# Kernel optimization log

Measured on AMD Instinct MI355X. Metric: run time of the kernel, lower is better.

## Reference

```python
import jax, jax.numpy as jnp
import numpy as np

B, H, W, C = 32, 64, 64, 64
F = 128
KH = KW = 3
SH = SW = 1
P = KH * KW * C  # flattened patch size = 576


def _glorot(key, shape):
    fan_in = KH * KW * C
    fan_out = KH * KW * F
    limit = np.sqrt(6.0 / (fan_in + fan_out)).astype(np.float32)
    return jax.random.uniform(key, shape, jnp.float32, -limit, limit)


def setup_inputs() -> dict:
    key = jax.random.key(0)
    k1, k2, k3 = jax.random.split(key, 3)
    inputs = jax.random.normal(k1, (B, H, W, C), dtype=jnp.float32)
    kernel = _glorot(k2, (KH, KW, C, F))
    control_points = _glorot(k3, (KH, KW, C, F))
    bias = jnp.zeros((F,), dtype=jnp.float32)
    return {"inputs": inputs, "kernel": kernel, "bias": bias, "control_points": control_points}


def _extract_patches(x):
    # SAME padding, stride 1; TF extract_patches ordering: (kh, kw, C), C fastest
    xp = jnp.pad(x, ((0, 0), (1, 1), (1, 1), (0, 0)))
    patches = jnp.stack(
        [xp[:, i:i + H, j:j + W, :] for i in range(KH) for j in range(KW)],
        axis=3,
    )  # [B, H, W, KH*KW, C]
    return patches.reshape(B, H, W, P)


def reference(inputs, kernel, bias, control_points):
    conv_out = jax.lax.conv_general_dilated(
        inputs, kernel, (SH, SW), "SAME",
        dimension_numbers=("NHWC", "HWIO", "NHWC"),
    )  # [B, H, W, F]

    # RBF branch via ||a-b||^2 = ||a||^2 + ||b||^2 - 2 a.b
    p = _extract_patches(inputs).reshape(-1, P)        # [N, P]
    c = control_points.reshape(P, F)                   # [P, F]
    pn = jnp.sum(p * p, axis=1, keepdims=True)         # [N, 1]
    cn = jnp.sum(c * c, axis=0)                        # [F]
    d = pn + cn - 2.0 * (p @ c)                        # [N, F] squared distances
    gamma = 1.0 / (2.0 * jnp.mean(d))                  # global mean over all patches/filters
    kan = jnp.exp(-gamma * d).reshape(B, H, W, F)

    return conv_out + kan + bias
```

## Files before the change

kernel.cpp:

```cpp
#include <hip/hip_runtime.h>


#define B_ 32
#define H_ 64
#define W_ 64
#define C_ 64
#define F_ 128
#define P_ 576
#define NPIX (B_*H_*W_)
#define NF   (NPIX*F_)

typedef __bf16  bf16x8 __attribute__((ext_vector_type(8)));
typedef float   f32x4  __attribute__((ext_vector_type(4)));

union FU  { float f; uint u; };
union BFU { __bf16 h; ushort s; };
union PKU { __bf16 h[2]; uint u; };

__device__ __forceinline__ ushort f2bf(float f) { BFU q; q.h = (__bf16)f; return q.s; }
__device__ __forceinline__ uint pk(float a, float b) {
    PKU q; q.h[0] = (__bf16)a; q.h[1] = (__bf16)b; return q.u;
}
__device__ __forceinline__ float bflo(uint u) { FU v; v.u = u << 16; return v.f; }
__device__ __forceinline__ float bfhi(uint u) { FU v; v.u = u & 0xffff0000u; return v.f; }

__device__ __forceinline__ void gll16(const void* g, void* l) {
    __builtin_amdgcn_global_load_lds((const __attribute__((address_space(1))) void*)g,
                                     (__attribute__((address_space(3))) void*)l, 16, 0, 0);
}

#define ACC_SPN 0
#define ACC_SPC 16
#define ACC_SCN 32

__global__ void k_prep(const float* __restrict__ wgt, const float* __restrict__ ctrl,
                       ushort* __restrict__ wsB, float* __restrict__ cn,
                       float* __restrict__ accum, float* __restrict__ tab) {
    __shared__ __attribute__((aligned(16))) float sh[1024];
    if (blockIdx.x < 288) {
        int e = blockIdx.x * 256 + threadIdx.x;
        int p = e >> 7, f = e & 127;
        int kc = p >> 6, r = p & 63;
        int ks = r >> 5, quad = (r >> 3) & 3, j = r & 7;
        int ntg = f >> 4, l16 = f & 15;
        int off0 = (kc * 2 + ks) * 8192 + ntg * 512 + (quad * 16 + l16) * 8 + j;
        wsB[off0]        = f2bf(wgt[e]);
        wsB[off0 + 4096] = f2bf(ctrl[e]);
    } else if (blockIdx.x == 288) {
        int t = threadIdx.x;
        int col = t & 31, pc = t >> 5;
        f32x4 a = {0.f, 0.f, 0.f, 0.f};
        const float* base = ctrl + col * 4;
        #pragma unroll 4
        for (int p = pc * 72; p < pc * 72 + 72; ++p) {
            f32x4 v = *(const f32x4*)(base + p * F_);
            a += v * v;
        }
        f32x4* sh4 = (f32x4*)sh;
        sh4[t] = a;
        __syncthreads();
        f32x4 s = {0.f, 0.f, 0.f, 0.f};
        if (t < 32) {
            #pragma unroll
            for (int q = 0; q < 8; ++q) s += sh4[q * 32 + t];
            *(f32x4*)(cn + t * 4) = s;
        }
        float tot = s.x + s.y + s.z + s.w;
        if (t < 64) {
            #pragma unroll
            for (int off = 32; off >= 1; off >>= 1) tot += __shfl_down(tot, off, 64);
            if (t == 0) {
                accum[ACC_SPN] = 0.f;
                accum[ACC_SPC] = 0.f;
                accum[ACC_SCN] = tot;
            }
        }
    } else {
        int t = threadIdx.x;
        for (int e = t; e < 576; e += 256) {
            const f32x4* row = (const f32x4*)(ctrl + e * F_);
            f32x4 a = {0.f, 0.f, 0.f, 0.f};
            #pragma unroll 8
            for (int q = 0; q < 32; ++q) a += row[q];
            sh[e] = a.x + a.y + a.z + a.w;
        }
        __syncthreads();
        for (int idx = t; idx < 576; idx += 256) {
            int q = idx >> 6, c = idx & 63;
            int ry = q / 3, rx = q - 3 * ry;
            int my = (ry == 0) ? 3 : (ry == 2) ? 6 : 7;
            int mx = (rx == 0) ? 3 : (rx == 2) ? 6 : 7;
            float s = 0.f;
            #pragma unroll
            for (int ki = 0; ki < 3; ++ki)
                #pragma unroll
                for (int kj = 0; kj < 3; ++kj)
                    if ((my >> ki & 1) && (mx >> kj & 1))
                        s += sh[(ki * 3 + kj) * 64 + c];
            tab[idx] = s;
        }
    }
}

__launch_bounds__(256)
__global__ void k_gamma(const float* __restrict__ in, const float* __restrict__ tab,
                        float* __restrict__ accum) {
    __shared__ float shs[4], shp[4];
    const int t = threadIdx.x, seg = t & 15, grp = t >> 4;
    float s = 0.f, pc = 0.f;
    #pragma unroll 4
    for (int it = 0; it < 16; ++it) {
        int pix = blockIdx.x * 256 + it * 16 + grp;
        int y = (pix >> 6) & 63, x = pix & 63;
        float4 v = *((const float4*)(in + pix * 64) + seg);
        int ry = (y == 0) ? 0 : (y == 63) ? 2 : 1;
        int rx = (x == 0) ? 0 : (x == 63) ? 2 : 1;
        float4 tv = *((const float4*)(tab + (ry * 3 + rx) * 64) + seg);
        float wq = (float)((3 - (y == 0) - (y == 63)) * (3 - (x == 0) - (x == 63)));
        s  += wq * (v.x*v.x + v.y*v.y + v.z*v.z + v.w*v.w);
        pc += v.x*tv.x + v.y*tv.y + v.z*tv.z + v.w*tv.w;
    }
    #pragma unroll
    for (int off = 32; off >= 1; off >>= 1) {
        s  += __shfl_down(s,  off, 64);
        pc += __shfl_down(pc, off, 64);
    }
    if ((t & 63) == 0) { shs[t >> 6] = s; shp[t >> 6] = pc; }
    __syncthreads();
    if (t == 0)  atomicAdd(&accum[ACC_SPN], shs[0] + shs[1] + shs[2] + shs[3]);
    if (t == 64) atomicAdd(&accum[ACC_SPC], shp[0] + shp[1] + shp[2] + shp[3]);
}

__launch_bounds__(512, 4)
__global__ void k_main(const float* __restrict__ in, const ushort* __restrict__ wsB,
                       const float* __restrict__ bias, const float* __restrict__ cn,
                       const float* __restrict__ accum, float* __restrict__ out) {
    __shared__ __attribute__((aligned(16))) ushort smem[34592];
    ushort* lI   = smem;
    ushort* lB   = smem + 17408;
    float*  sArr = (float*)(smem + 33792);
    float*  pnAr = (float*)(smem + 34336);

    const int tid = threadIdx.x;
    const int n0  = blockIdx.x * 128;
    const int b   = n0 >> 12;
    const int y0  = (n0 >> 6) & 63;
    const float* inb = in + b * 262144;

    const int w     = tid >> 6, lane = tid & 63;
    const int fq    = w & 3, mhalf = w >> 2;
    const int quad  = lane >> 4, l16 = lane & 15;

    {
        const char* src = (const char*)wsB + tid * 16;
        char* dst = (char*)lB + tid * 16;
        gll16(src, dst);
        gll16(src + 8192, dst + 8192);
    }

    for (int g = tid; g < 2176; g += 512) {
        int row4 = g / 544;
        int rem  = g - row4 * 544;
        int px = rem >> 3, c = rem & 7;
        int y = y0 + row4 - 1, x = px - 1;
        float4 v0 = make_float4(0.f, 0.f, 0.f, 0.f), v1 = v0;
        if (y >= 0 && y < 64 && x >= 0 && x < 64) {
            const float* sp = inb + y * 4096 + x * 64 + c * 8;
            v0 = *(const float4*)sp;
            v1 = *(const float4*)(sp + 4);
        }
        uint4 o = { pk(v0.x, v0.y), pk(v0.z, v0.w), pk(v1.x, v1.y), pk(v1.z, v1.w) };
        *(uint4*)&lI[(row4 * 68 + px) * 64 + ((c ^ (px & 7)) << 3)] = o;
    }
    __syncthreads();

    for (int g = tid; g < 264; g += 512) {
        int row4 = g / 66, px = g - row4 * 66;
        const ushort* base = &lI[(row4 * 68 + px) * 64];
        float s = 0.f;
        #pragma unroll
        for (int j = 0; j < 8; ++j) {
            int jj = (j + px) & 7;
            uint4 v = *(const uint4*)&base[jj << 3];
            float a0 = bflo(v.x), a1 = bfhi(v.x), a2 = bflo(v.y), a3 = bfhi(v.y);
            float a4 = bflo(v.z), a5 = bfhi(v.z), a6 = bflo(v.w), a7 = bfhi(v.w);
            s += a0*a0 + a1*a1 + a2*a2 + a3*a3 + a4*a4 + a5*a5 + a6*a6 + a7*a7;
        }
        sArr[row4 * 66 == 0 ? 0 : 0] = 0.f;
        sArr[row4 * 68 + px] = s;
    }
    __syncthreads();

    if (tid < 128) {
        int yr = tid >> 6, x = tid & 63;
        float a = 0.f;
        #pragma unroll
        for (int dr = 0; dr < 3; ++dr)
            #pragma unroll
            for (int dc = 0; dc < 3; ++dc)
                a += sArr[(yr + dr) * 68 + x + dc];
        pnAr[tid] = a;
    }

    f32x4 accW[4][2], accC[4][2];
    #pragma unroll
    for (int mt = 0; mt < 4; ++mt)
        #pragma unroll
        for (int nt = 0; nt < 2; ++nt) {
            accW[mt][nt] = (f32x4){0.f, 0.f, 0.f, 0.f};
            accC[mt][nt] = (f32x4){0.f, 0.f, 0.f, 0.f};
        }

    const int fq2 = fq * 2;
    int cur = 0;
    #pragma unroll 1
    for (int t18 = 0; t18 < 18; ++t18) {
        const int kc = t18 >> 1, ks = t18 & 1;
        const int ki = (kc >= 6) ? 2 : (kc >= 3) ? 1 : 0;
        const int kj = kc - 3 * ki;

        if (t18 < 17) {
            const char* src = (const char*)wsB + (t18 + 1) * 16384 + tid * 16;
            char* dst = (char*)lB + ((cur ^ 1) * 16384) + tid * 16;
            gll16(src, dst);
            gll16(src + 8192, dst + 8192);
        }

        const ushort* lBc = lB + cur * 8192;
        bf16x8 bw[2], bc[2];
        #pragma unroll
        for (int nt = 0; nt < 2; ++nt) {
            bw[nt] = *(const bf16x8*)&lBc[(fq2 + nt) * 512 + lane * 8];
            bc[nt] = *(const bf16x8*)&lBc[4096 + (fq2 + nt) * 512 + lane * 8];
        }
        const int swk = (l16 + kj) & 7;
        const int rb0 = (mhalf + ki) * 68 + l16 + kj;
        const int sw  = ((ks * 4 + quad) ^ swk) << 3;
        #pragma unroll
        for (int mt = 0; mt < 4; ++mt) {
            bf16x8 a = *(const bf16x8*)&lI[(rb0 + mt * 16) * 64 + sw];
            #pragma unroll
            for (int nt = 0; nt < 2; ++nt) {
                accW[mt][nt] = __builtin_amdgcn_mfma_f32_16x16x32_bf16(a, bw[nt], accW[mt][nt], 0, 0, 0);
                accC[mt][nt] = __builtin_amdgcn_mfma_f32_16x16x32_bf16(a, bc[nt], accC[mt][nt], 0, 0, 0);
            }
        }
        __syncthreads();
        cur ^= 1;
    }

    float Spn = accum[ACC_SPN], Spc = accum[ACC_SPC], Scn = accum[ACC_SCN];
    float Sd  = 128.f * Spn + 131072.f * Scn - 2.f * Spc;
    float g   = 0.5f * 16777216.f / Sd;
    float bv[2], cv[2];
    #pragma unroll
    for (int nt = 0; nt < 2; ++nt) {
        int gf = fq * 32 + nt * 16 + l16;
        bv[nt] = bias[gf];
        cv[nt] = cn[gf];
    }
    #pragma unroll
    for (int mt = 0; mt < 4; ++mt) {
        int rloc = mhalf * 64 + mt * 16 + quad * 4;
        float pv[4];
        #pragma unroll
        for (int r = 0; r < 4; ++r) pv[r] = pnAr[rloc + r];
        int gm = n0 + rloc;
        #pragma unroll
        for (int nt = 0; nt < 2; ++nt) {
            int gf = fq * 32 + nt * 16 + l16;
            #pragma unroll
            for (int r = 0; r < 4; ++r) {
                float d = pv[r] + cv[nt] - 2.f * accC[mt][nt][r];
                out[(gm + r) * F_ + gf] = accW[mt][nt][r] + bv[nt] + __expf(-g * d);
            }
        }
    }
}

extern "C" void kernel_launch(void* const* d_in, const int* in_sizes, int n_in,
                              void* d_out, int out_size, void* d_ws, size_t ws_size,
                              hipStream_t stream) {
    const float* in   = (const float*)d_in[0];
    const float* wgt  = (const float*)d_in[1];
    const float* bias = (const float*)d_in[2];
    const float* ctrl = (const float*)d_in[3];
    float* out = (float*)d_out;

    char* ws = (char*)d_ws;
    ushort* wsB   = (ushort*)(ws + 0);
    float*  cn    = (float*) (ws + 294912);
    float*  accum = (float*) (ws + 295424);
    float*  tab   = (float*) (ws + 295616);

    k_prep  <<<290,        256, 0, stream>>>(wgt, ctrl, wsB, cn, accum, tab);
    k_gamma <<<NPIX / 256, 256, 0, stream>>>(in, tab, accum);
    k_main  <<<NPIX / 128, 512, 0, stream>>>(in, wsB, bias, cn, accum, out);
}
```

Measured before the change: 146.8 us.

## Fuse gamma reduction into prep kernel and replace atomics with per-block partials

Merges the gamma-statistics kernel into the prep kernel as extra blocks, so one launch goes away. Each stats block now rebuilds the border table in LDS and writes per-block partial sums instead of doing atomics, and the main kernel reduces all 512 partials itself. The main kernel also computes the per-pixel squared norms during the LDS fill using shuffles, which removes a separate LDS pass and barrier. It skips the final-iteration barrier and raises wave priority around the MFMA block. The cost is that every stats block recomputes the 576-entry table redundantly, and every main wave reads 1024 partials.

```diff
diff --git a/kernel.cpp b/kernel.cpp
--- a/kernel.cpp
+++ b/kernel.cpp
@@ -13,7 +13,6 @@
 typedef __bf16  bf16x8 __attribute__((ext_vector_type(8)));
 typedef float   f32x4  __attribute__((ext_vector_type(4)));
 
-union FU  { float f; uint u; };
 union BFU { __bf16 h; ushort s; };
 union PKU { __bf16 h[2]; uint u; };
 
@@ -21,24 +20,23 @@
 __device__ __forceinline__ uint pk(float a, float b) {
     PKU q; q.h[0] = (__bf16)a; q.h[1] = (__bf16)b; return q.u;
 }
-__device__ __forceinline__ float bflo(uint u) { FU v; v.u = u << 16; return v.f; }
-__device__ __forceinline__ float bfhi(uint u) { FU v; v.u = u & 0xffff0000u; return v.f; }
 
 __device__ __forceinline__ void gll16(const void* g, void* l) {
     __builtin_amdgcn_global_load_lds((const __attribute__((address_space(1))) void*)g,
                                      (__attribute__((address_space(3))) void*)l, 16, 0, 0);
 }
 
-#define ACC_SPN 0
-#define ACC_SPC 16
-#define ACC_SCN 32
-
-__global__ void k_prep(const float* __restrict__ wgt, const float* __restrict__ ctrl,
-                       ushort* __restrict__ wsB, float* __restrict__ cn,
-                       float* __restrict__ accum, float* __restrict__ tab) {
+__global__ void k_prep(const float* __restrict__ in, const float* __restrict__ wgt,
+                       const float* __restrict__ ctrl, ushort* __restrict__ wsB,
+                       float* __restrict__ cn, float* __restrict__ accum,
+                       float* __restrict__ spn, float* __restrict__ spc) {
     __shared__ __attribute__((aligned(16))) float sh[1024];
+    __shared__ float tabL[576];
+    __shared__ float shs[4], shp[4];
+    const int t = threadIdx.x;
+
     if (blockIdx.x < 288) {
-        int e = blockIdx.x * 256 + threadIdx.x;
+        int e = blockIdx.x * 256 + t;
         int p = e >> 7, f = e & 127;
         int kc = p >> 6, r = p & 63;
         int ks = r >> 5, quad = (r >> 3) & 3, j = r & 7;
@@ -46,13 +44,14 @@
         int off0 = (kc * 2 + ks) * 8192 + ntg * 512 + (quad * 16 + l16) * 8 + j;
         wsB[off0]        = f2bf(wgt[e]);
         wsB[off0 + 4096] = f2bf(ctrl[e]);
-    } else if (blockIdx.x == 288) {
-        int t = threadIdx.x;
-        int col = t & 31, pc = t >> 5;
+        return;
+    }
+    if (blockIdx.x == 288) {
+        int col = t & 31, pc8 = t >> 5;
         f32x4 a = {0.f, 0.f, 0.f, 0.f};
         const float* base = ctrl + col * 4;
         #pragma unroll 4
-        for (int p = pc * 72; p < pc * 72 + 72; ++p) {
+        for (int p = pc8 * 72; p < pc8 * 72 + 72; ++p) {
             f32x4 v = *(const f32x4*)(base + p * F_);
             a += v * v;
         }
@@ -69,53 +68,46 @@
         if (t < 64) {
             #pragma unroll
             for (int off = 32; off >= 1; off >>= 1) tot += __shfl_down(tot, off, 64);
-            if (t == 0) {
-                accum[ACC_SPN] = 0.f;
-                accum[ACC_SPC] = 0.f;
-                accum[ACC_SCN] = tot;
-            }
-        }
-    } else {
-        int t = threadIdx.x;
-        for (int e = t; e < 576; e += 256) {
-            const f32x4* row = (const f32x4*)(ctrl + e * F_);
-            f32x4 a = {0.f, 0.f, 0.f, 0.f};
-            #pragma unroll 8
-            for (int q = 0; q < 32; ++q) a += row[q];
-            sh[e] = a.x + a.y + a.z + a.w;
-        }
-        __syncthreads();
-        for (int idx = t; idx < 576; idx += 256) {
-            int q = idx >> 6, c = idx & 63;
-            int ry = q / 3, rx = q - 3 * ry;
-            int my = (ry == 0) ? 3 : (ry == 2) ? 6 : 7;
-            int mx = (rx == 0) ? 3 : (rx == 2) ? 6 : 7;
-            float s = 0.f;
-            #pragma unroll
-            for (int ki = 0; ki < 3; ++ki)
-                #pragma unroll
-                for (int kj = 0; kj < 3; ++kj)
-                    if ((my >> ki & 1) && (mx >> kj & 1))
-                        s += sh[(ki * 3 + kj) * 64 + c];
-            tab[idx] = s;
-        }
-    }
-}
-
-__launch_bounds__(256)
-__global__ void k_gamma(const float* __restrict__ in, const float* __restrict__ tab,
-                        float* __restrict__ accum) {
-    __shared__ float shs[4], shp[4];
-    const int t = threadIdx.x, seg = t & 15, grp = t >> 4;
+            if (t == 0) accum[0] = tot;
+        }
+        return;
+    }
+
+    const int sb = blockIdx.x - 289;
+    for (int e = t; e < 576; e += 256) {
+        const f32x4* row = (const f32x4*)(ctrl + e * F_);
+        f32x4 a = {0.f, 0.f, 0.f, 0.f};
+        #pragma unroll 8
+        for (int q = 0; q < 32; ++q) a += row[q];
+        sh[e] = a.x + a.y + a.z + a.w;
+    }
+    __syncthreads();
+    for (int idx = t; idx < 576; idx += 256) {
+        int q = idx >> 6, c = idx & 63;
+        int ry = q / 3, rx = q - 3 * ry;
+        int my = (ry == 0) ? 3 : (ry == 2) ? 6 : 7;
+        int mx = (rx == 0) ? 3 : (rx == 2) ? 6 : 7;
+        float s = 0.f;
+        #pragma unroll
+        for (int ki = 0; ki < 3; ++ki)
+            #pragma unroll
+            for (int kj = 0; kj < 3; ++kj)
+                if ((my >> ki & 1) && (mx >> kj & 1))
+                    s += sh[(ki * 3 + kj) * 64 + c];
+        tabL[idx] = s;
+    }
+    __syncthreads();
+
+    const int seg = t & 15, grp = t >> 4;
     float s = 0.f, pc = 0.f;
     #pragma unroll 4
     for (int it = 0; it < 16; ++it) {
-        int pix = blockIdx.x * 256 + it * 16 + grp;
+        int pix = sb * 256 + it * 16 + grp;
         int y = (pix >> 6) & 63, x = pix & 63;
         float4 v = *((const float4*)(in + pix * 64) + seg);
         int ry = (y == 0) ? 0 : (y == 63) ? 2 : 1;
         int rx = (x == 0) ? 0 : (x == 63) ? 2 : 1;
-        float4 tv = *((const float4*)(tab + (ry * 3 + rx) * 64) + seg);
+        float4 tv = *((const float4*)(tabL + (ry * 3 + rx) * 64) + seg);
         float wq = (float)((3 - (y == 0) - (y == 63)) * (3 - (x == 0) - (x == 63)));
         s  += wq * (v.x*v.x + v.y*v.y + v.z*v.z + v.w*v.w);
         pc += v.x*tv.x + v.y*tv.y + v.z*tv.z + v.w*tv.w;
@@ -127,14 +119,15 @@
     }
     if ((t & 63) == 0) { shs[t >> 6] = s; shp[t >> 6] = pc; }
     __syncthreads();
-    if (t == 0)  atomicAdd(&accum[ACC_SPN], shs[0] + shs[1] + shs[2] + shs[3]);
-    if (t == 64) atomicAdd(&accum[ACC_SPC], shp[0] + shp[1] + shp[2] + shp[3]);
+    if (t == 0)  spn[sb] = shs[0] + shs[1] + shs[2] + shs[3];
+    if (t == 64) spc[sb] = shp[0] + shp[1] + shp[2] + shp[3];
 }
 
 __launch_bounds__(512, 4)
 __global__ void k_main(const float* __restrict__ in, const ushort* __restrict__ wsB,
                        const float* __restrict__ bias, const float* __restrict__ cn,
-                       const float* __restrict__ accum, float* __restrict__ out) {
+                       const float* __restrict__ accum, const float* __restrict__ spn,
+                       const float* __restrict__ spc, float* __restrict__ out) {
     __shared__ __attribute__((aligned(16))) ushort smem[34592];
     ushort* lI   = smem;
     ushort* lB   = smem + 17408;
@@ -171,23 +164,12 @@
         }
         uint4 o = { pk(v0.x, v0.y), pk(v0.z, v0.w), pk(v1.x, v1.y), pk(v1.z, v1.w) };
         *(uint4*)&lI[(row4 * 68 + px) * 64 + ((c ^ (px & 7)) << 3)] = o;
-    }
-    __syncthreads();
-
-    for (int g = tid; g < 264; g += 512) {
-        int row4 = g / 66, px = g - row4 * 66;
-        const ushort* base = &lI[(row4 * 68 + px) * 64];
-        float s = 0.f;
-        #pragma unroll
-        for (int j = 0; j < 8; ++j) {
-            int jj = (j + px) & 7;
-            uint4 v = *(const uint4*)&base[jj << 3];
-            float a0 = bflo(v.x), a1 = bfhi(v.x), a2 = bflo(v.y), a3 = bfhi(v.y);
-            float a4 = bflo(v.z), a5 = bfhi(v.z), a6 = bflo(v.w), a7 = bfhi(v.w);
-            s += a0*a0 + a1*a1 + a2*a2 + a3*a3 + a4*a4 + a5*a5 + a6*a6 + a7*a7;
-        }
-        sArr[row4 * 66 == 0 ? 0 : 0] = 0.f;
-        sArr[row4 * 68 + px] = s;
+        float s8 = v0.x*v0.x + v0.y*v0.y + v0.z*v0.z + v0.w*v0.w
+                 + v1.x*v1.x + v1.y*v1.y + v1.z*v1.z + v1.w*v1.w;
+        s8 += __shfl_xor(s8, 1, 64);
+        s8 += __shfl_xor(s8, 2, 64);
+        s8 += __shfl_xor(s8, 4, 64);
+        if ((g & 7) == 0) sArr[row4 * 68 + px] = s8;
     }
     __syncthreads();
 
@@ -236,6 +218,7 @@
         const int swk = (l16 + kj) & 7;
         const int rb0 = (mhalf + ki) * 68 + l16 + kj;
         const int sw  = ((ks * 4 + quad) ^ swk) << 3;
+        __builtin_amdgcn_s_setprio(1);
         #pragma unroll
         for (int mt = 0; mt < 4; ++mt) {
             bf16x8 a = *(const bf16x8*)&lI[(rb0 + mt * 16) * 64 + sw];
@@ -245,13 +228,24 @@
                 accC[mt][nt] = __builtin_amdgcn_mfma_f32_16x16x32_bf16(a, bc[nt], accC[mt][nt], 0, 0, 0);
             }
         }
-        __syncthreads();
+        __builtin_amdgcn_s_setprio(0);
+        if (t18 < 17) __syncthreads();
         cur ^= 1;
     }
 
-    float Spn = accum[ACC_SPN], Spc = accum[ACC_SPC], Scn = accum[ACC_SCN];
-    float Sd  = 128.f * Spn + 131072.f * Scn - 2.f * Spc;
-    float g   = 0.5f * 16777216.f / Sd;
+    float sp = 0.f, sc = 0.f;
+    #pragma unroll
+    for (int q = 0; q < 8; ++q) {
+        sp += spn[q * 64 + lane];
+        sc += spc[q * 64 + lane];
+    }
+    #pragma unroll
+    for (int off = 32; off >= 1; off >>= 1) {
+        sp += __shfl_xor(sp, off, 64);
+        sc += __shfl_xor(sc, off, 64);
+    }
+    float Sd = 128.f * sp + 131072.f * accum[0] - 2.f * sc;
+    float g  = 0.5f * 16777216.f / Sd;
     float bv[2], cv[2];
     #pragma unroll
     for (int nt = 0; nt < 2; ++nt) {
@@ -291,9 +285,9 @@
     ushort* wsB   = (ushort*)(ws + 0);
     float*  cn    = (float*) (ws + 294912);
     float*  accum = (float*) (ws + 295424);
-    float*  tab   = (float*) (ws + 295616);
-
-    k_prep  <<<290,        256, 0, stream>>>(wgt, ctrl, wsB, cn, accum, tab);
-    k_gamma <<<NPIX / 256, 256, 0, stream>>>(in, tab, accum);
-    k_main  <<<NPIX / 128, 512, 0, stream>>>(in, wsB, bias, cn, accum, out);
-}
+    float*  spn   = (float*) (ws + 295488);
+    float*  spc   = (float*) (ws + 297536);
+
+    k_prep <<<801,        256, 0, stream>>>(in, wgt, ctrl, wsB, cn, accum, spn, spc);
+    k_main <<<NPIX / 128, 512, 0, stream>>>(in, wsB, bias, cn, accum, spn, spc, out);
+}
```

Measured after the change: 150.5 us. 1.03x slower.
